# Kernel tuning notes

Measured on AMD Instinct MI355X. Metric: run time of the kernel, lower is better.

## Reference

```python
import jax, jax.numpy as jnp
import numpy as np

N = 10000      # num_nodes
RP = 16        # latent relations
E = 64         # emb_dim
R = 8000       # num triples (MLP input dim)
NT = 8000      # unique (s,o) pairs (unique by construction)
LW = 64        # lwidth
C = 16         # num_classes
NREL = 50      # num_rels (<= R columns actually used in nhots)


def setup_inputs() -> dict:
    rng = np.random.default_rng(0)
    # unique (s,o) pairs -> nt == R, deterministic shapes
    pair_ids = rng.choice(N * N, size=R, replace=False)
    s = (pair_ids // N).astype(np.int32)
    o = (pair_ids % N).astype(np.int32)
    p = rng.integers(0, NREL, size=R)
    nhots = np.zeros((NT, R), np.float32)
    nhots[np.arange(NT), p] = 1.0
    # replicate index construction from __init__ exactly
    rm = np.arange(RP, dtype=np.int32)[:, None]           # (RP,1)
    s_exp = np.broadcast_to(s[None, :], (RP, NT)).reshape(-1)
    o_exp = np.broadcast_to(o[None, :], (RP, NT)).reshape(-1)
    se = (s[None, :] * rm).reshape(-1)
    oe = (o[None, :] * rm).reshape(-1)
    hindices = np.stack([s_exp, oe], axis=1).astype(np.int32)  # into (N, N*RP)
    vindices = np.stack([se, o_exp], axis=1).astype(np.int32)  # into (N*RP, N)

    key = jax.random.key(0)
    ks = jax.random.split(key, 6)
    inv = lambda d: 1.0 / np.sqrt(d)
    return {
        'nhots': jnp.asarray(nhots),
        'w1a': jax.random.normal(ks[0], (R, LW), jnp.float32) * inv(R),
        'b1a': jnp.zeros((LW,), jnp.float32),
        'w1b': jax.random.normal(ks[1], (LW, RP), jnp.float32) * inv(LW),
        'b1b': jnp.zeros((RP,), jnp.float32),
        'w2a': jax.random.normal(ks[2], (R, LW), jnp.float32) * inv(R),
        'b2a': jnp.zeros((LW,), jnp.float32),
        'w2b': jax.random.normal(ks[3], (LW, RP), jnp.float32) * inv(LW),
        'b2b': jnp.zeros((RP,), jnp.float32),
        'weights1': jax.random.normal(ks[4], (RP, N, E), jnp.float32) * 0.02,
        'bias1': jnp.zeros((E,), jnp.float32),
        'weights2': jax.random.normal(ks[5], (RP, E, C), jnp.float32) * 0.02,
        'bias2': jnp.zeros((C,), jnp.float32),
        'hindices': jnp.asarray(hindices),
        'vindices': jnp.asarray(vindices),
    }


def _latents(nhots, wa, ba, wb, bb):
    # Linear -> ReLU -> Linear -> softmax over rp, then .t().reshape(-1)
    lat = jax.nn.softmax(jax.nn.relu(nhots @ wa + ba) @ wb + bb, axis=1)  # (NT, RP)
    return lat.T.reshape(-1)  # (RP*NT,) — rm-major, matching index construction


def reference(nhots, w1a, b1a, w1b, b1b, w2a, b2a, w2b, b2b,
              weights1, bias1, weights2, bias2, hindices, vindices):
    hrow, hcol = hindices[:, 0], hindices[:, 1]
    vrow, vcol = vindices[:, 0], vindices[:, 1]

    # --- layer 1: A1 (N, N*RP), column-normalized ---
    lat1 = _latents(nhots, w1a, b1a, w1b, b1b)
    colsum = jax.ops.segment_sum(lat1, hcol, num_segments=N * RP)
    lat1 = lat1 / colsum[hcol]
    Xw = weights1.reshape(RP * N, E)
    h = jax.ops.segment_sum(lat1[:, None] * Xw[hcol], hrow, num_segments=N)  # (N, E)
    h = jax.nn.relu(h + bias1)

    # --- layer 2: A2 (N*RP, N), row-normalized ---
    lat2 = _latents(nhots, w2a, b2a, w2b, b2b)
    rowsum = jax.ops.segment_sum(lat2, vrow, num_segments=N * RP)
    lat2 = lat2 / rowsum[vrow]
    h2 = jax.ops.segment_sum(lat2[:, None] * h[vcol], vrow, num_segments=N * RP)
    h2 = h2.reshape(RP, N, E)

    out = jnp.einsum('rhc,rnh->nc', weights2, h2) + bias2  # (N, C)
    return out
```

## Files before the change

kernel.cpp:

```cpp
#include <hip/hip_runtime.h>
#include <hip/hip_bf16.h>


#define N_     10000
#define RP_    16
#define E_     64
#define R_     8000
#define NT_    8000
#define C_     16
#define NE_    128000

#define WS_ZERO_FLOATS 960064

__global__ void k_init_out(float* __restrict__ out, const float* __restrict__ bias2) {
    int i = blockIdx.x * 256 + threadIdx.x;
    out[i] = bias2[i & 15];
}

__global__ void k_lat(const float* __restrict__ nhots,
                      const float* __restrict__ w1a, const float* __restrict__ b1a,
                      const float* __restrict__ w1b, const float* __restrict__ b1b,
                      const float* __restrict__ w2a, const float* __restrict__ b2a,
                      const float* __restrict__ w2b, const float* __restrict__ b2b,
                      float* __restrict__ lat1, float* __restrict__ lat2) {
    __shared__ float zb[4][128];
    const int lane = threadIdx.x & 63;
    const int wv   = threadIdx.x >> 6;
    const int t    = blockIdx.x * 4 + wv;

    const float4 v = reinterpret_cast<const float4*>(nhots + (size_t)t * R_)[lane];
    float acc1 = 0.f, acc2 = 0.f;
    const float comp[4] = {v.x, v.y, v.z, v.w};
    #pragma unroll
    for (int c = 0; c < 4; ++c) {
        unsigned long long m = __ballot(comp[c] != 0.0f);
        while (m) {
            const int src = __ffsll(m) - 1;
            m &= m - 1;
            const float val = __shfl(comp[c], src);
            const int col = src * 4 + c;
            acc1 += val * w1a[col * 64 + lane];
            acc2 += val * w2a[col * 64 + lane];
        }
    }
    zb[wv][lane]      = fmaxf(acc1 + b1a[lane], 0.f);
    zb[wv][64 + lane] = fmaxf(acc2 + b2a[lane], 0.f);
    __syncthreads();

    const int g = lane >> 4, r = lane & 15;
    float pre = 0.f;
    if (g < 2) {
        const float* wb = (g == 0) ? w1b : w2b;
        pre = ((g == 0) ? b1b : b2b)[r];
        const float* z = &zb[wv][g * 64];
        #pragma unroll
        for (int l = 0; l < 64; ++l) pre += z[l] * wb[l * 16 + r];
    }
    float mx = pre;
    #pragma unroll
    for (int m = 8; m >= 1; m >>= 1) mx = fmaxf(mx, __shfl_xor(mx, m, 16));
    const float e = expf(pre - mx);
    float s = e;
    #pragma unroll
    for (int m = 8; m >= 1; m >>= 1) s += __shfl_xor(s, m, 16);
    const float lt = e / s;
    if (g == 0)      lat1[r * NT_ + t] = lt;
    else if (g == 1) lat2[r * NT_ + t] = lt;
}

__global__ void k_sum(const float* __restrict__ lat1, const float* __restrict__ lat2,
                      const int* __restrict__ hind, const int* __restrict__ vind,
                      float* __restrict__ colsum, float* __restrict__ rowsum) {
    const int k = blockIdx.x * 256 + threadIdx.x;
    const int lane = threadIdx.x & 63;

    {
        const float a = lat1[k];
        const int key = hind[2 * k + 1];
        const int k0 = __shfl(key, 0);
        if (__all(key == k0)) {
            float vsum = a;
            #pragma unroll
            for (int m = 32; m >= 1; m >>= 1) vsum += __shfl_xor(vsum, m);
            if (lane == 0) atomicAdd(colsum + k0, vsum);
        } else {
            atomicAdd(colsum + key, a);
        }
    }
    {
        const float b = lat2[k];
        const int key = vind[2 * k];
        const int k0 = __shfl(key, 0);
        if (__all(key == k0)) {
            float vsum = b;
            #pragma unroll
            for (int m = 32; m >= 1; m >>= 1) vsum += __shfl_xor(vsum, m);
            if (lane == 0) atomicAdd(rowsum + k0, vsum);
        } else {
            atomicAdd(rowsum + key, b);
        }
    }
}

__global__ void k_h(const float* __restrict__ lat1, const float* __restrict__ colsum,
                    const int* __restrict__ hind, const float* __restrict__ w1full,
                    float* __restrict__ hbuf) {
    const int gid = blockIdx.x * 256 + threadIdx.x;
    const int k = gid >> 6;
    const int l = gid & 63;
    const int ck = hind[2 * k + 1];
    const int rw = hind[2 * k];
    const float a = lat1[k] / colsum[ck];
    atomicAdd(&hbuf[rw * 64 + l], a * w1full[ck * 64 + l]);
}

__global__ void k_hrelu(float* __restrict__ hbuf, const float* __restrict__ bias1) {
    const int i = blockIdx.x * 256 + threadIdx.x;
    hbuf[i] = fmaxf(hbuf[i] + bias1[i & 63], 0.f);
}

__global__ void k_h2r0(const float* __restrict__ lat2, const float* __restrict__ rowsum,
                       const int* __restrict__ vind, const float* __restrict__ hbuf,
                       float* __restrict__ h2r0) {
    const int l  = threadIdx.x & 63;
    const int wg = blockIdx.x * 4 + (threadIdx.x >> 6);
    float acc = 0.f;
    for (int t = wg; t < NT_; t += 256) {
        const int vc = vind[2 * t + 1];
        acc += lat2[t] * hbuf[vc * 64 + l];
    }
    acc /= rowsum[0];
    atomicAdd(&h2r0[l], acc);
}

__global__ void k_h2r0b(const float* __restrict__ h2r0, const float* __restrict__ w2,
                        float* __restrict__ out) {
    const int c = threadIdx.x;
    if (c < 16) {
        float acc = 0.f;
        #pragma unroll
        for (int hh = 0; hh < 64; ++hh) acc += w2[hh * 16 + c] * h2r0[hh];
        atomicAdd(&out[c], acc);
    }
}

__global__ void k_h2out(const float* __restrict__ lat2, const float* __restrict__ rowsum,
                        const int* __restrict__ vind, const float* __restrict__ hbuf,
                        const float* __restrict__ w2, float* __restrict__ out) {
    __shared__ float sw2[16384];
    for (int i = threadIdx.x; i < 16384; i += 256) sw2[i] = w2[i];
    __syncthreads();
    const int grp = (threadIdx.x >> 4) & 3;
    for (int gid = blockIdx.x * 256 + threadIdx.x; gid < 120000 * 16; gid += gridDim.x * 256) {
        const int e = gid >> 4;
        const int c = gid & 15;
        const int k = NT_ + e;
        const int q  = vind[2 * k];
        const int vc = vind[2 * k + 1];
        const float val = lat2[k] / rowsum[q];
        const int rp = q / N_;
        const int np = q - rp * N_;
        const float* wrow = &sw2[rp * 1024 + c];
        const float* hrow = &hbuf[vc * 64];
        float acc = 0.f;
        for (int hh = grp; hh < 64; ++hh) acc += wrow[hh * 16] * hrow[hh];
        for (int hh = 0; hh < grp; ++hh)  acc += wrow[hh * 16] * hrow[hh];
        atomicAdd(&out[np * 16 + c], val * acc);
    }
}

extern "C" void kernel_launch(void* const* d_in, const int* in_sizes, int n_in,
                              void* d_out, int out_size, void* d_ws, size_t ws_size,
                              hipStream_t stream) {
    const float* nhots    = (const float*)d_in[0];
    const float* w1a      = (const float*)d_in[1];
    const float* b1a      = (const float*)d_in[2];
    const float* w1b      = (const float*)d_in[3];
    const float* b1b      = (const float*)d_in[4];
    const float* w2a      = (const float*)d_in[5];
    const float* b2a      = (const float*)d_in[6];
    const float* w2b      = (const float*)d_in[7];
    const float* b2b      = (const float*)d_in[8];
    const float* weights1 = (const float*)d_in[9];
    const float* bias1    = (const float*)d_in[10];
    const float* weights2 = (const float*)d_in[11];
    const float* bias2    = (const float*)d_in[12];
    const int*   hind     = (const int*)d_in[13];
    const int*   vind     = (const int*)d_in[14];
    float* out = (float*)d_out;

    float* ws     = (float*)d_ws;
    float* colsum = ws;
    float* rowsum = ws + 160000;
    float* hbuf   = ws + 320000;
    float* h2r0   = ws + 960000;
    float* lat1   = ws + 960064;
    float* lat2   = ws + 1088064;

    hipMemsetAsync(d_ws, 0, WS_ZERO_FLOATS * sizeof(float), stream);
    k_init_out<<<625, 256, 0, stream>>>(out, bias2);
    k_lat<<<2000, 256, 0, stream>>>(nhots, w1a, b1a, w1b, b1b, w2a, b2a, w2b, b2b, lat1, lat2);
    k_sum<<<500, 256, 0, stream>>>(lat1, lat2, hind, vind, colsum, rowsum);
    k_h<<<32000, 256, 0, stream>>>(lat1, colsum, hind, weights1, hbuf);
    k_hrelu<<<2500, 256, 0, stream>>>(hbuf, bias1);
    k_h2r0<<<64, 256, 0, stream>>>(lat2, rowsum, vind, hbuf, h2r0);
    k_h2out<<<512, 256, 0, stream>>>(lat2, rowsum, vind, hbuf, weights2, out);
    k_h2r0b<<<1, 64, 0, stream>>>(h2r0, weights2, out);
}
```

Measured before the change: 516.5 us.

## Replace atomic scatter for layer-1 with CSR gather and fuse normalizer sums

Folds the column/row normalizer sums into the latent kernel, so the separate pass over the latent arrays goes away. Layer 1 previously used 8M float atomics into hbuf; it now builds a CSR grouping of triples by subject node (count, single-block scan, scatter) and gathers per node with one wavefront, applying bias and ReLU in the same pass. The zeroed workspace shrinks because hbuf no longer needs clearing, and the h2out grid is doubled. The price is three extra small launches, including a single-block scan, and nondeterministic ordering in the scatter.

```diff
diff --git a/kernel.cpp b/kernel.cpp
--- a/kernel.cpp
+++ b/kernel.cpp
@@ -10,7 +10,7 @@
 #define C_     16
 #define NE_    128000
 
-#define WS_ZERO_FLOATS 960064
+#define WS_ZERO_UNITS 330064
 
 __global__ void k_init_out(float* __restrict__ out, const float* __restrict__ bias2) {
     int i = blockIdx.x * 256 + threadIdx.x;
@@ -22,8 +22,12 @@
                       const float* __restrict__ w1b, const float* __restrict__ b1b,
                       const float* __restrict__ w2a, const float* __restrict__ b2a,
                       const float* __restrict__ w2b, const float* __restrict__ b2b,
-                      float* __restrict__ lat1, float* __restrict__ lat2) {
+                      const int* __restrict__ hind, const int* __restrict__ vind,
+                      float* __restrict__ lat1t, float* __restrict__ lat2,
+                      float* __restrict__ colsum, float* __restrict__ rowsum,
+                      int* __restrict__ cnt) {
     __shared__ float zb[4][128];
+    __shared__ float r0[2];
     const int lane = threadIdx.x & 63;
     const int wv   = threadIdx.x >> 6;
     const int t    = blockIdx.x * 4 + wv;
@@ -43,6 +47,7 @@
             acc2 += val * w2a[col * 64 + lane];
         }
     }
+    if (threadIdx.x == 0) { r0[0] = 0.f; r0[1] = 0.f; }
     zb[wv][lane]      = fmaxf(acc1 + b1a[lane], 0.f);
     zb[wv][64 + lane] = fmaxf(acc2 + b2a[lane], 0.f);
     __syncthreads();
@@ -64,59 +69,83 @@
     #pragma unroll
     for (int m = 8; m >= 1; m >>= 1) s += __shfl_xor(s, m, 16);
     const float lt = e / s;
-    if (g == 0)      lat1[r * NT_ + t] = lt;
-    else if (g == 1) lat2[r * NT_ + t] = lt;
-}
-
-__global__ void k_sum(const float* __restrict__ lat1, const float* __restrict__ lat2,
-                      const int* __restrict__ hind, const int* __restrict__ vind,
-                      float* __restrict__ colsum, float* __restrict__ rowsum) {
-    const int k = blockIdx.x * 256 + threadIdx.x;
+
+    const int s_t = hind[2 * t];
+    const int o_t = vind[2 * t + 1];
+    if (g == 0) {
+        lat1t[t * 16 + r] = lt;
+        if (r) atomicAdd(colsum + o_t * r, lt);
+        else   atomicAdd(&r0[0], lt);
+    } else if (g == 1) {
+        lat2[r * NT_ + t] = lt;
+        if (r) atomicAdd(rowsum + s_t * r, lt);
+        else   atomicAdd(&r0[1], lt);
+    } else if (g == 2 && r == 0) {
+        atomicAdd(cnt + s_t, 1);
+    }
+    __syncthreads();
+    if (threadIdx.x == 0) atomicAdd(colsum, r0[0]);
+    if (threadIdx.x == 1) atomicAdd(rowsum, r0[1]);
+}
+
+__global__ void k_scan(const int* __restrict__ cnt, int* __restrict__ off,
+                       int* __restrict__ woff) {
+    __shared__ int sh[1024];
+    const int i = threadIdx.x;
+    int local[10];
+    int sum = 0;
+    const int base = i * 10;
+    #pragma unroll
+    for (int j = 0; j < 10; ++j) {
+        const int idx = base + j;
+        const int c = (idx < N_) ? cnt[idx] : 0;
+        local[j] = c; sum += c;
+    }
+    sh[i] = sum;
+    __syncthreads();
+    for (int d = 1; d < 1024; d <<= 1) {
+        const int v = (i >= d) ? sh[i - d] : 0;
+        __syncthreads();
+        sh[i] += v;
+        __syncthreads();
+    }
+    int run = sh[i] - sum;
+    #pragma unroll
+    for (int j = 0; j < 10; ++j) {
+        const int idx = base + j;
+        if (idx < N_) { off[idx] = run; woff[idx] = run; run += local[j]; }
+    }
+    if (i == 1023) off[N_] = sh[1023];
+}
+
+__global__ void k_scatter(const int* __restrict__ hind, int* __restrict__ woff,
+                          int* __restrict__ order) {
+    const int t = blockIdx.x * 64 + threadIdx.x;
+    const int n = hind[2 * t];
+    const int pos = atomicAdd(woff + n, 1);
+    order[pos] = t;
+}
+
+__global__ void k_hg(const float* __restrict__ lat1t, const float* __restrict__ colsum,
+                     const int* __restrict__ off, const int* __restrict__ order,
+                     const int* __restrict__ vind, const float* __restrict__ w1,
+                     const float* __restrict__ bias1, float* __restrict__ hbuf) {
     const int lane = threadIdx.x & 63;
-
-    {
-        const float a = lat1[k];
-        const int key = hind[2 * k + 1];
-        const int k0 = __shfl(key, 0);
-        if (__all(key == k0)) {
-            float vsum = a;
-            #pragma unroll
-            for (int m = 32; m >= 1; m >>= 1) vsum += __shfl_xor(vsum, m);
-            if (lane == 0) atomicAdd(colsum + k0, vsum);
-        } else {
-            atomicAdd(colsum + key, a);
+    const int n = blockIdx.x * 4 + (threadIdx.x >> 6);
+    const int j1 = off[n + 1];
+    float acc = 0.f;
+    for (int j = off[n]; j < j1; ++j) {
+        const int t = order[j];
+        const int o_t = vind[2 * t + 1];
+        float ln = 0.f;
+        if (lane < 16) ln = lat1t[t * 16 + lane] / colsum[o_t * lane];
+        #pragma unroll
+        for (int r = 0; r < 16; ++r) {
+            const float a = __shfl(ln, r);
+            acc += a * w1[(o_t * r) * 64 + lane];
         }
     }
-    {
-        const float b = lat2[k];
-        const int key = vind[2 * k];
-        const int k0 = __shfl(key, 0);
-        if (__all(key == k0)) {
-            float vsum = b;
-            #pragma unroll
-            for (int m = 32; m >= 1; m >>= 1) vsum += __shfl_xor(vsum, m);
-            if (lane == 0) atomicAdd(rowsum + k0, vsum);
-        } else {
-            atomicAdd(rowsum + key, b);
-        }
-    }
-}
-
-__global__ void k_h(const float* __restrict__ lat1, const float* __restrict__ colsum,
-                    const int* __restrict__ hind, const float* __restrict__ w1full,
-                    float* __restrict__ hbuf) {
-    const int gid = blockIdx.x * 256 + threadIdx.x;
-    const int k = gid >> 6;
-    const int l = gid & 63;
-    const int ck = hind[2 * k + 1];
-    const int rw = hind[2 * k];
-    const float a = lat1[k] / colsum[ck];
-    atomicAdd(&hbuf[rw * 64 + l], a * w1full[ck * 64 + l]);
-}
-
-__global__ void k_hrelu(float* __restrict__ hbuf, const float* __restrict__ bias1) {
-    const int i = blockIdx.x * 256 + threadIdx.x;
-    hbuf[i] = fmaxf(hbuf[i] + bias1[i & 63], 0.f);
+    hbuf[n * 64 + lane] = fmaxf(acc + bias1[lane], 0.f);
 }
 
 __global__ void k_h2r0(const float* __restrict__ lat2, const float* __restrict__ rowsum,
@@ -192,18 +221,23 @@
     float* ws     = (float*)d_ws;
     float* colsum = ws;
     float* rowsum = ws + 160000;
-    float* hbuf   = ws + 320000;
-    float* h2r0   = ws + 960000;
-    float* lat1   = ws + 960064;
-    float* lat2   = ws + 1088064;
-
-    hipMemsetAsync(d_ws, 0, WS_ZERO_FLOATS * sizeof(float), stream);
+    float* h2r0   = ws + 320000;
+    int*   cnt    = (int*)(ws + 320064);
+    int*   off    = (int*)(ws + 330064);
+    int*   woff   = (int*)(ws + 340065);
+    int*   order  = (int*)(ws + 350065);
+    float* hbuf   = ws + 358080;
+    float* lat1t  = ws + 998080;
+    float* lat2   = ws + 1126080;
+
+    hipMemsetAsync(d_ws, 0, WS_ZERO_UNITS * sizeof(float), stream);
     k_init_out<<<625, 256, 0, stream>>>(out, bias2);
-    k_lat<<<2000, 256, 0, stream>>>(nhots, w1a, b1a, w1b, b1b, w2a, b2a, w2b, b2b, lat1, lat2);
-    k_sum<<<500, 256, 0, stream>>>(lat1, lat2, hind, vind, colsum, rowsum);
-    k_h<<<32000, 256, 0, stream>>>(lat1, colsum, hind, weights1, hbuf);
-    k_hrelu<<<2500, 256, 0, stream>>>(hbuf, bias1);
+    k_lat<<<2000, 256, 0, stream>>>(nhots, w1a, b1a, w1b, b1b, w2a, b2a, w2b, b2b,
+                                    hind, vind, lat1t, lat2, colsum, rowsum, cnt);
+    k_scan<<<1, 1024, 0, stream>>>(cnt, off, woff);
+    k_scatter<<<125, 64, 0, stream>>>(hind, woff, order);
+    k_hg<<<2500, 256, 0, stream>>>(lat1t, colsum, off, order, vind, weights1, bias1, hbuf);
     k_h2r0<<<64, 256, 0, stream>>>(lat2, rowsum, vind, hbuf, h2r0);
-    k_h2out<<<512, 256, 0, stream>>>(lat2, rowsum, vind, hbuf, weights2, out);
+    k_h2out<<<1024, 256, 0, stream>>>(lat2, rowsum, vind, hbuf, weights2, out);
     k_h2r0b<<<1, 64, 0, stream>>>(h2r0, weights2, out);
 }
```

New measurement: 515.5 us. No clear change (-0.2%).
